# Kernel optimization log

Hardware: AMD Instinct MI355X
Metric: run time of the kernel (lower is better)

Reference implementation:

```python
import jax, jax.numpy as jnp
import numpy as np

B, L, F = 64, 65536, 32  # batch, signal length, deep_feature_dim


def setup_inputs() -> dict:
    key = jax.random.key(0)
    ks = jax.random.split(key, 11)
    s = 0.05
    return {
        "x": jax.random.normal(ks[0], (B, L), dtype=jnp.float32),
        "conv_w": jax.random.normal(ks[1], (F, 1, 3), dtype=jnp.float32) * s,
        "conv_b": jax.random.normal(ks[2], (F,), dtype=jnp.float32) * s,
        "w1": jax.random.normal(ks[3], (F + 4, 64), dtype=jnp.float32) * s,
        "b1": jax.random.normal(ks[4], (64,), dtype=jnp.float32) * s,
        "w2": jax.random.normal(ks[5], (64, 32), dtype=jnp.float32) * s,
        "b2": jax.random.normal(ks[6], (32,), dtype=jnp.float32) * s,
        "w3": jax.random.normal(ks[7], (32, 16), dtype=jnp.float32) * s,
        "b3": jax.random.normal(ks[8], (16,), dtype=jnp.float32) * s,
        "w4": jax.random.normal(ks[9], (16, 2), dtype=jnp.float32) * s,
        "b4": jax.random.normal(ks[10], (2,), dtype=jnp.float32) * s,
    }


def reference(x, conv_w, conv_b, w1, b1, w2, b2, w3, b3, w4, b4):
    # knowledge-driven stats over the length axis (population variance, ddof=0)
    mean = jnp.mean(x, axis=1)
    var = jnp.mean(jnp.square(x - mean[:, None]), axis=1)
    mx = jnp.max(x, axis=1)
    mn = jnp.min(x, axis=1)
    kd = jnp.stack([mean, var, mx, mn], axis=1)  # [B, 4]

    # deep extractor: Conv1d(1->F, k=3, pad=1) + ReLU + global max pool
    xc = x[:, None, :]  # [B, 1, L]
    conv = jax.lax.conv_general_dilated(
        xc, conv_w, window_strides=(1,), padding=[(1, 1)],
        dimension_numbers=("NCH", "OIH", "NCH"))  # [B, F, L]
    conv = jax.nn.relu(conv + conv_b[None, :, None])
    deep = jnp.max(conv, axis=-1)  # [B, F]

    h = jnp.concatenate([deep, kd], axis=1)  # [B, F+4]
    h = jax.nn.relu(h @ w1 + b1)
    h = jax.nn.relu(h @ w2 + b2)
    h = jax.nn.relu(h @ w3 + b3)
    return h @ w4 + b4  # [B, 2]
```

## Files before the change

kernel.cpp:

```cpp
#include <hip/hip_runtime.h>

#define L_LEN  65536
#define B_ROWS 64
#define NF     32
#define SLICES 32
#define TPB    256
#define CHUNK  (L_LEN / SLICES)
#define EPT    (CHUNK / TPB)
#define NV     36

__global__ __launch_bounds__(TPB) void fp_pass1(
    const float* __restrict__ x, const float* __restrict__ cw,
    float* __restrict__ ws)
{
    const int row   = blockIdx.x;
    const int slice = blockIdx.y;
    const float* xr = x + (size_t)row * L_LEN;
    const int base  = slice * CHUNK + (int)threadIdx.x * EPT;

    float xv[EPT + 2];
    const float4* p = reinterpret_cast<const float4*>(xr + base);
    float4 a = p[0];
    float4 b = p[1];
    xv[1] = a.x; xv[2] = a.y; xv[3] = a.z; xv[4] = a.w;
    xv[5] = b.x; xv[6] = b.y; xv[7] = b.z; xv[8] = b.w;
    xv[0]       = (base == 0)            ? 0.0f : xr[base - 1];
    xv[EPT + 1] = (base + EPT == L_LEN)  ? 0.0f : xr[base + EPT];

    float s = 0.0f, ss = 0.0f;
    float mx = -3.4e38f, mn = 3.4e38f;
#pragma unroll
    for (int j = 1; j <= EPT; ++j) {
        const float v = xv[j];
        s += v;
        ss = fmaf(v, v, ss);
        mx = fmaxf(mx, v);
        mn = fminf(mn, v);
    }

    float m[NF];
#pragma unroll
    for (int f = 0; f < NF; ++f) {
        const float w0 = cw[3 * f + 0];
        const float w1 = cw[3 * f + 1];
        const float w2 = cw[3 * f + 2];
        float best0 = -3.4e38f, best1 = -3.4e38f;
#pragma unroll
        for (int j = 0; j < EPT; j += 2) {
            const float c0 = fmaf(w0, xv[j],     fmaf(w1, xv[j + 1], w2 * xv[j + 2]));
            const float c1 = fmaf(w0, xv[j + 1], fmaf(w1, xv[j + 2], w2 * xv[j + 3]));
            best0 = fmaxf(best0, c0);
            best1 = fmaxf(best1, c1);
        }
        m[f] = fmaxf(best0, best1);
    }

#pragma unroll
    for (int off = 32; off > 0; off >>= 1) {
        s  += __shfl_xor(s,  off, 64);
        ss += __shfl_xor(ss, off, 64);
        mx  = fmaxf(mx, __shfl_xor(mx, off, 64));
        mn  = fminf(mn, __shfl_xor(mn, off, 64));
#pragma unroll
        for (int f = 0; f < NF; ++f)
            m[f] = fmaxf(m[f], __shfl_xor(m[f], off, 64));
    }

    __shared__ float red[TPB / 64][NV];
    const int wid  = threadIdx.x >> 6;
    const int lane = threadIdx.x & 63;
    if (lane == 0) {
        red[wid][0] = s; red[wid][1] = ss; red[wid][2] = mx; red[wid][3] = mn;
#pragma unroll
        for (int f = 0; f < NF; ++f) red[wid][4 + f] = m[f];
    }
    __syncthreads();
    if (threadIdx.x < NV) {
        const int v = threadIdx.x;
        float r;
        if (v < 2)
            r = (red[0][v] + red[1][v]) + (red[2][v] + red[3][v]);
        else if (v == 3)
            r = fminf(fminf(red[0][v], red[1][v]), fminf(red[2][v], red[3][v]));
        else
            r = fmaxf(fmaxf(red[0][v], red[1][v]), fmaxf(red[2][v], red[3][v]));
        ws[((size_t)row * SLICES + slice) * NV + v] = r;
    }
}

__global__ __launch_bounds__(64) void fp_pass2(
    const float* __restrict__ ws, const float* __restrict__ cb,
    const float* __restrict__ w1, const float* __restrict__ b1,
    const float* __restrict__ w2, const float* __restrict__ b2,
    const float* __restrict__ w3, const float* __restrict__ b3,
    const float* __restrict__ w4, const float* __restrict__ b4,
    float* __restrict__ out)
{
    const int row = blockIdx.x;
    const int t   = (int)threadIdx.x;
    __shared__ float feat[NV];
    __shared__ float h1[64];
    __shared__ float h2[32];
    __shared__ float h3[16];

    if (t < NV) {
        const float* p = ws + (size_t)row * SLICES * NV + t;
        float r = p[0];
        if (t < 2) {
            for (int sl = 1; sl < SLICES; ++sl) r += p[sl * NV];
        } else if (t == 3) {
            for (int sl = 1; sl < SLICES; ++sl) r = fminf(r, p[sl * NV]);
        } else {
            for (int sl = 1; sl < SLICES; ++sl) r = fmaxf(r, p[sl * NV]);
        }
        if (t >= 4)       feat[t - 4] = fmaxf(r + cb[t - 4], 0.0f);
        else if (t == 2)  feat[34] = r;
        else if (t == 3)  feat[35] = r;
        else              feat[32 + t] = r;
    }
    __syncthreads();
    if (t == 0) {
        const float inv = 1.0f / (float)L_LEN;
        const float mean = feat[32] * inv;
        const float var  = feat[33] * inv - mean * mean;
        feat[32] = mean;
        feat[33] = var;
    }
    __syncthreads();

    {
        float acc = b1[t];
        for (int i = 0; i < NV; ++i) acc = fmaf(feat[i], w1[i * 64 + t], acc);
        h1[t] = fmaxf(acc, 0.0f);
    }
    __syncthreads();
    if (t < 32) {
        float acc = b2[t];
        for (int i = 0; i < 64; ++i) acc = fmaf(h1[i], w2[i * 32 + t], acc);
        h2[t] = fmaxf(acc, 0.0f);
    }
    __syncthreads();
    if (t < 16) {
        float acc = b3[t];
        for (int i = 0; i < 32; ++i) acc = fmaf(h2[i], w3[i * 16 + t], acc);
        h3[t] = fmaxf(acc, 0.0f);
    }
    __syncthreads();
    if (t < 2) {
        float acc = b4[t];
        for (int i = 0; i < 16; ++i) acc = fmaf(h3[i], w4[i * 2 + t], acc);
        out[row * 2 + t] = acc;
    }
}

extern "C" void kernel_launch(void* const* d_in, const int* in_sizes, int n_in,
                              void* d_out, int out_size, void* d_ws, size_t ws_size,
                              hipStream_t stream) {
    const float* x  = (const float*)d_in[0];
    const float* cw = (const float*)d_in[1];
    const float* cb = (const float*)d_in[2];
    const float* w1 = (const float*)d_in[3];
    const float* b1 = (const float*)d_in[4];
    const float* w2 = (const float*)d_in[5];
    const float* b2 = (const float*)d_in[6];
    const float* w3 = (const float*)d_in[7];
    const float* b3 = (const float*)d_in[8];
    const float* w4 = (const float*)d_in[9];
    const float* b4 = (const float*)d_in[10];
    float* out = (float*)d_out;
    float* ws  = (float*)d_ws;

    dim3 g1(B_ROWS, SLICES);
    fp_pass1<<<g1, TPB, 0, stream>>>(x, cw, ws);
    fp_pass2<<<B_ROWS, 64, 0, stream>>>(ws, cb, w1, b1, w2, b2, w3, b3, w4, b4, out);
}
```

Measured before the change: 109.4 us.

## Halve slices, vectorize conv with packed float2 FMA, reduce via shared memory

Cuts slices per row from 32 to 16, so each thread handles 16 elements instead of 8 and halo overhead drops. The conv and stats loops use float2 vectors so the compiler can emit packed FP32 FMA instructions. The 36-value shuffle-xor butterfly is replaced by a padded shared-memory transpose in which 144 threads each reduce a strided column and then finish with two shuffles. This trades shuffle traffic for a larger LDS footprint and fewer blocks, which may lower occupancy.

```diff
diff --git a/kernel.cpp b/kernel.cpp
--- a/kernel.cpp
+++ b/kernel.cpp
@@ -3,11 +3,14 @@
 #define L_LEN  65536
 #define B_ROWS 64
 #define NF     32
-#define SLICES 32
+#define SLICES 16
 #define TPB    256
 #define CHUNK  (L_LEN / SLICES)
 #define EPT    (CHUNK / TPB)
 #define NV     36
+#define PAD    37
+
+typedef float f2 __attribute__((ext_vector_type(2)));
 
 __global__ __launch_bounds__(TPB) void fp_pass1(
     const float* __restrict__ x, const float* __restrict__ cw,
@@ -15,76 +18,83 @@
 {
     const int row   = blockIdx.x;
     const int slice = blockIdx.y;
+    const int t     = (int)threadIdx.x;
     const float* xr = x + (size_t)row * L_LEN;
-    const int base  = slice * CHUNK + (int)threadIdx.x * EPT;
+    const int base  = slice * CHUNK + t * EPT;
 
     float xv[EPT + 2];
     const float4* p = reinterpret_cast<const float4*>(xr + base);
-    float4 a = p[0];
-    float4 b = p[1];
-    xv[1] = a.x; xv[2] = a.y; xv[3] = a.z; xv[4] = a.w;
-    xv[5] = b.x; xv[6] = b.y; xv[7] = b.z; xv[8] = b.w;
-    xv[0]       = (base == 0)            ? 0.0f : xr[base - 1];
-    xv[EPT + 1] = (base + EPT == L_LEN)  ? 0.0f : xr[base + EPT];
+    float4 a0 = p[0], a1 = p[1], a2 = p[2], a3 = p[3];
+    xv[1]  = a0.x; xv[2]  = a0.y; xv[3]  = a0.z; xv[4]  = a0.w;
+    xv[5]  = a1.x; xv[6]  = a1.y; xv[7]  = a1.z; xv[8]  = a1.w;
+    xv[9]  = a2.x; xv[10] = a2.y; xv[11] = a2.z; xv[12] = a2.w;
+    xv[13] = a3.x; xv[14] = a3.y; xv[15] = a3.z; xv[16] = a3.w;
+    xv[0]           = (base == 0)           ? 0.0f : xr[base - 1];
+    xv[EPT + 1]     = (base + EPT == L_LEN) ? 0.0f : xr[base + EPT];
 
-    float s = 0.0f, ss = 0.0f;
-    float mx = -3.4e38f, mn = 3.4e38f;
+    f2 ev[EPT / 2 + 1], od[EPT / 2];
 #pragma unroll
-    for (int j = 1; j <= EPT; ++j) {
-        const float v = xv[j];
-        s += v;
-        ss = fmaf(v, v, ss);
-        mx = fmaxf(mx, v);
-        mn = fminf(mn, v);
+    for (int i = 0; i <= EPT / 2; ++i) ev[i] = f2{xv[2 * i], xv[2 * i + 1]};
+#pragma unroll
+    for (int i = 0; i < EPT / 2; ++i)  od[i] = f2{xv[2 * i + 1], xv[2 * i + 2]};
+
+    f2 s2 = f2{0.0f, 0.0f}, ss2 = f2{0.0f, 0.0f};
+#pragma unroll
+    for (int i = 0; i < EPT / 2; ++i) {
+        s2 += od[i];
+        ss2 = __builtin_elementwise_fma(od[i], od[i], ss2);
+    }
+    float s  = s2.x + s2.y;
+    float ss = ss2.x + ss2.y;
+    float mx = xv[1], mn = xv[1];
+#pragma unroll
+    for (int j = 2; j <= EPT; ++j) {
+        mx = fmaxf(mx, xv[j]);
+        mn = fminf(mn, xv[j]);
     }
 
     float m[NF];
 #pragma unroll
     for (int f = 0; f < NF; ++f) {
-        const float w0 = cw[3 * f + 0];
-        const float w1 = cw[3 * f + 1];
-        const float w2 = cw[3 * f + 2];
+        const f2 w0 = f2{cw[3 * f + 0], cw[3 * f + 0]};
+        const f2 w1 = f2{cw[3 * f + 1], cw[3 * f + 1]};
+        const f2 w2 = f2{cw[3 * f + 2], cw[3 * f + 2]};
         float best0 = -3.4e38f, best1 = -3.4e38f;
 #pragma unroll
-        for (int j = 0; j < EPT; j += 2) {
-            const float c0 = fmaf(w0, xv[j],     fmaf(w1, xv[j + 1], w2 * xv[j + 2]));
-            const float c1 = fmaf(w0, xv[j + 1], fmaf(w1, xv[j + 2], w2 * xv[j + 3]));
-            best0 = fmaxf(best0, c0);
-            best1 = fmaxf(best1, c1);
+        for (int i = 0; i < EPT / 2; i += 2) {
+            f2 c0 = __builtin_elementwise_fma(w0, ev[i],
+                     __builtin_elementwise_fma(w1, od[i], w2 * ev[i + 1]));
+            f2 c1 = __builtin_elementwise_fma(w0, ev[i + 1],
+                     __builtin_elementwise_fma(w1, od[i + 1], w2 * ev[i + 2]));
+            best0 = fmaxf(best0, fmaxf(c0.x, c0.y));
+            best1 = fmaxf(best1, fmaxf(c1.x, c1.y));
         }
         m[f] = fmaxf(best0, best1);
     }
 
+    __shared__ float mred[TPB * PAD];
+    float* myrow = &mred[t * PAD];
+    myrow[0] = s; myrow[1] = ss; myrow[2] = mx; myrow[3] = mn;
 #pragma unroll
-    for (int off = 32; off > 0; off >>= 1) {
-        s  += __shfl_xor(s,  off, 64);
-        ss += __shfl_xor(ss, off, 64);
-        mx  = fmaxf(mx, __shfl_xor(mx, off, 64));
-        mn  = fminf(mn, __shfl_xor(mn, off, 64));
-#pragma unroll
-        for (int f = 0; f < NF; ++f)
-            m[f] = fmaxf(m[f], __shfl_xor(m[f], off, 64));
-    }
+    for (int f = 0; f < NF; ++f) myrow[4 + f] = m[f];
+    __syncthreads();
 
-    __shared__ float red[TPB / 64][NV];
-    const int wid  = threadIdx.x >> 6;
-    const int lane = threadIdx.x & 63;
-    if (lane == 0) {
-        red[wid][0] = s; red[wid][1] = ss; red[wid][2] = mx; red[wid][3] = mn;
-#pragma unroll
-        for (int f = 0; f < NF; ++f) red[wid][4 + f] = m[f];
-    }
-    __syncthreads();
-    if (threadIdx.x < NV) {
-        const int v = threadIdx.x;
-        float r;
-        if (v < 2)
-            r = (red[0][v] + red[1][v]) + (red[2][v] + red[3][v]);
-        else if (v == 3)
-            r = fminf(fminf(red[0][v], red[1][v]), fminf(red[2][v], red[3][v]));
-        else
-            r = fmaxf(fmaxf(red[0][v], red[1][v]), fmaxf(red[2][v], red[3][v]));
-        ws[((size_t)row * SLICES + slice) * NV + v] = r;
+    if (t < NV * 4) {
+        const int v = t >> 2, g = t & 3;
+        float rs = 0.0f, rmx = -3.4e38f, rmn = 3.4e38f;
+        for (int k = 0; k < TPB / 4; ++k) {
+            const float val = mred[(g + 4 * k) * PAD + v];
+            rs += val;
+            rmx = fmaxf(rmx, val);
+            rmn = fminf(rmn, val);
+        }
+        float r = (v < 2) ? rs : ((v == 3) ? rmn : rmx);
+        float o = __shfl_xor(r, 1, 64);
+        r = (v < 2) ? r + o : ((v == 3) ? fminf(r, o) : fmaxf(r, o));
+        o = __shfl_xor(r, 2, 64);
+        r = (v < 2) ? r + o : ((v == 3) ? fminf(r, o) : fmaxf(r, o));
+        if (g == 0)
+            ws[((size_t)(row * SLICES + slice)) * NV + v] = r;
     }
 }
 
@@ -105,14 +115,14 @@
 
     if (t < NV) {
         const float* p = ws + (size_t)row * SLICES * NV + t;
-        float r = p[0];
-        if (t < 2) {
-            for (int sl = 1; sl < SLICES; ++sl) r += p[sl * NV];
-        } else if (t == 3) {
-            for (int sl = 1; sl < SLICES; ++sl) r = fminf(r, p[sl * NV]);
-        } else {
-            for (int sl = 1; sl < SLICES; ++sl) r = fmaxf(r, p[sl * NV]);
+        float rs = 0.0f, rmx = -3.4e38f, rmn = 3.4e38f;
+        for (int sl = 0; sl < SLICES; ++sl) {
+            const float val = p[sl * NV];
+            rs += val;
+            rmx = fmaxf(rmx, val);
+            rmn = fminf(rmn, val);
         }
+        const float r = (t < 2) ? rs : ((t == 3) ? rmn : rmx);
         if (t >= 4)       feat[t - 4] = fmaxf(r + cb[t - 4], 0.0f);
         else if (t == 2)  feat[34] = r;
         else if (t == 3)  feat[35] = r;
@@ -120,7 +130,7 @@
     }
     __syncthreads();
     if (t == 0) {
-        const float inv = 1.0f / (float)L_LEN;
+        const float inv  = 1.0f / (float)L_LEN;
         const float mean = feat[32] * inv;
         const float var  = feat[33] * inv - mean * mean;
         feat[32] = mean;
```

Result: faster. 95.33 us (-12.8%).
